# Performance work log

Hardware: AMD Instinct MI355X
Metric: run time of the kernel (lower is better)

The kernel has to match this reference:

```python
import jax, jax.numpy as jnp
import numpy as np

# irreps "64x0e + 32x1o + 16x2e": dims 64*1 + 32*3 + 16*5 = 240
MUL = (64, 32, 16)
DEG = (1, 3, 5)  # 2l+1 for l=0,1,2
IRREPS_DIM = sum(m * d for m, d in zip(MUL, DEG))  # 240
N_NODES = 20000
N_EDGES = 320000


def equivariant_linear(x, W0, W1, W2):
    """e3nn-style linear: per-irrep channel mixing shared across m-components,
    with 1/sqrt(fan_in) path normalization."""
    ws = (W0, W1, W2)
    outs = []
    off = 0
    for (mul, deg, W) in zip(MUL, DEG, ws):
        blk = x[:, off:off + mul * deg].reshape(-1, mul, deg)  # (N, mul, 2l+1)
        y = jnp.einsum('oi,nid->nod', W, blk) / jnp.sqrt(jnp.asarray(mul, x.dtype))
        outs.append(y.reshape(-1, mul * deg))
        off += mul * deg
    return jnp.concatenate(outs, axis=-1)


def setup_inputs() -> dict:
    key = jax.random.key(0)
    k1, k2, k3, k4, k5, k6 = jax.random.split(key, 6)
    messages = jax.random.normal(k1, (N_EDGES, IRREPS_DIM), dtype=jnp.float32)
    edge_index = jax.random.randint(k2, (N_EDGES, 2), 0, N_NODES, dtype=jnp.int64)
    edge_cutoff = jax.random.uniform(k3, (N_EDGES,), dtype=jnp.float32)
    W0 = jax.random.normal(k4, (64, 64), dtype=jnp.float32)
    W1 = jax.random.normal(k5, (32, 32), dtype=jnp.float32)
    W2 = jax.random.normal(k6, (16, 16), dtype=jnp.float32)
    return {"messages": messages, "edge_index": edge_index, "edge_cutoff": edge_cutoff,
            "W0": W0, "W1": W1, "W2": W2, "n_nodes": N_NODES}


def reference(messages, edge_index, edge_cutoff, W0, W1, W2, n_nodes):
    target = edge_index[:, 1]
    weighted = messages * edge_cutoff[:, None]  # fused cutoff multiply
    agg = jax.ops.segment_sum(weighted, target, num_segments=n_nodes)  # (n_nodes, 240)
    return equivariant_linear(agg, W0, W1, W2)
```

## Files before the change

kernel.cpp:

```cpp
#include <hip/hip_runtime.h>

#define IRREPS 240
#define NPB 4

__global__ void histogram_kernel(const int* __restrict__ eidx, int* __restrict__ counts,
                                 int n_edges) {
    int e = blockIdx.x * blockDim.x + threadIdx.x;
    if (e >= n_edges) return;
    int2 p = reinterpret_cast<const int2*>(eidx)[e];
    atomicAdd(&counts[p.y], 1);
}

__global__ void scan_kernel(const int* __restrict__ counts, int* __restrict__ offsets,
                            int* __restrict__ cursor, int n) {
    __shared__ int part[1024];
    int t = threadIdx.x;
    int per = (n + 1023) / 1024;
    int start = t * per;
    int end = min(start + per, n);
    int sum = 0;
    for (int i = start; i < end; ++i) sum += counts[i];
    part[t] = sum;
    __syncthreads();
    for (int off = 1; off < 1024; off <<= 1) {
        int v = (t >= off) ? part[t - off] : 0;
        __syncthreads();
        part[t] += v;
        __syncthreads();
    }
    int run = (t == 0) ? 0 : part[t - 1];
    for (int i = start; i < end; ++i) {
        offsets[i] = run;
        cursor[i] = run;
        run += counts[i];
    }
}

__global__ void fill_kernel(const int* __restrict__ eidx, int* __restrict__ cursor,
                            int* __restrict__ edge_ids, int n_edges) {
    int e = blockIdx.x * blockDim.x + threadIdx.x;
    if (e >= n_edges) return;
    int2 p = reinterpret_cast<const int2*>(eidx)[e];
    int pos = atomicAdd(&cursor[p.y], 1);
    edge_ids[pos] = e;
}

__global__ void gather_linear_kernel(const float* __restrict__ msgs,
                                     const float* __restrict__ cutoff,
                                     const int* __restrict__ edge_ids,
                                     const int* __restrict__ offsets,
                                     const int* __restrict__ counts,
                                     const float* __restrict__ W0,
                                     const float* __restrict__ W1,
                                     const float* __restrict__ W2,
                                     float* __restrict__ out,
                                     int n_nodes) {
    __shared__ float s_node[NPB][IRREPS];

    int t = threadIdx.x;
    int w = t >> 6;
    int lane = t & 63;
    int n = blockIdx.x * NPB + w;

    float4 acc = make_float4(0.f, 0.f, 0.f, 0.f);

    if (n < n_nodes) {
        int beg = offsets[n];
        int cnt = counts[n];
        for (int base = 0; base < cnt; base += 64) {
            int bn = min(64, cnt - base);
            int myeid = 0;
            float myw = 0.f;
            if (lane < bn) {
                myeid = edge_ids[beg + base + lane];
                myw = cutoff[myeid];
            }
            #pragma unroll 8
            for (int j = 0; j < bn; ++j) {
                int e = __shfl(myeid, j);
                float wgt = __shfl(myw, j);
                if (lane < 60) {
                    const float4 m = *reinterpret_cast<const float4*>(
                        msgs + (long long)e * IRREPS + lane * 4);
                    acc.x += m.x * wgt;
                    acc.y += m.y * wgt;
                    acc.z += m.z * wgt;
                    acc.w += m.w * wgt;
                }
            }
        }
    }

    if (lane < 60) {
        *reinterpret_cast<float4*>(&s_node[w][lane * 4]) = acc;
    }
    __syncthreads();

    for (int j = 0; j < NPB; ++j) {
        int nd = blockIdx.x * NPB + j;
        if (nd >= n_nodes) break;
        if (t < IRREPS) {
            const float* s = s_node[j];
            float a = 0.f;
            float res;
            if (t < 64) {
                int o = t;
                #pragma unroll 8
                for (int i = 0; i < 64; ++i) a += W0[o * 64 + i] * s[i];
                res = a * 0.125f;
            } else if (t < 160) {
                int rel = t - 64;
                int o = rel / 3, d = rel % 3;
                #pragma unroll 8
                for (int i = 0; i < 32; ++i) a += W1[o * 32 + i] * s[64 + i * 3 + d];
                res = a * 0.17677669529663687f;
            } else {
                int rel = t - 160;
                int o = rel / 5, d = rel % 5;
                #pragma unroll
                for (int i = 0; i < 16; ++i) a += W2[o * 16 + i] * s[160 + i * 5 + d];
                res = a * 0.25f;
            }
            out[(long long)nd * IRREPS + t] = res;
        }
    }
}

extern "C" void kernel_launch(void* const* d_in, const int* in_sizes, int n_in,
                              void* d_out, int out_size, void* d_ws, size_t ws_size,
                              hipStream_t stream) {
    const float* msgs   = (const float*)d_in[0];
    const int*   eidx   = (const int*)d_in[1];
    const float* cutoff = (const float*)d_in[2];
    const float* W0     = (const float*)d_in[3];
    const float* W1     = (const float*)d_in[4];
    const float* W2     = (const float*)d_in[5];

    int n_edges = in_sizes[0] / IRREPS;
    int n_nodes = out_size / IRREPS;

    int* counts   = (int*)d_ws;
    int* offsets  = counts + n_nodes;
    int* cursor   = offsets + n_nodes;
    int* edge_ids = cursor + n_nodes;

    hipMemsetAsync(counts, 0, (size_t)n_nodes * sizeof(int), stream);

    int block = 256;
    int egrid = (n_edges + block - 1) / block;
    histogram_kernel<<<egrid, block, 0, stream>>>(eidx, counts, n_edges);
    scan_kernel<<<1, 1024, 0, stream>>>(counts, offsets, cursor, n_nodes);
    fill_kernel<<<egrid, block, 0, stream>>>(eidx, cursor, edge_ids, n_edges);

    int ngrid = (n_nodes + NPB - 1) / NPB;
    gather_linear_kernel<<<ngrid, 256, 0, stream>>>(
        msgs, cutoff, edge_ids, offsets, counts, W0, W1, W2, (float*)d_out, n_nodes);
}
```

Before: 183.9 us.

## Pre-permute weighted messages into CSR order as bf16 before reduction

New measurement: 236.2 us. 28.4% more time.

```diff
diff --git a/kernel.cpp b/kernel.cpp
--- a/kernel.cpp
+++ b/kernel.cpp
@@ -1,6 +1,8 @@
 #include <hip/hip_runtime.h>
+#include <hip/hip_bf16.h>
 
 #define IRREPS 240
+#define ROWPAD 256
 #define NPB 4
 
 __global__ void histogram_kernel(const int* __restrict__ eidx, int* __restrict__ counts,
@@ -36,18 +38,43 @@
     }
 }
 
-__global__ void fill_kernel(const int* __restrict__ eidx, int* __restrict__ cursor,
-                            int* __restrict__ edge_ids, int n_edges) {
+__global__ void fill_slot_kernel(const int* __restrict__ eidx, int* __restrict__ cursor,
+                                 int* __restrict__ slot, int n_edges) {
     int e = blockIdx.x * blockDim.x + threadIdx.x;
     if (e >= n_edges) return;
     int2 p = reinterpret_cast<const int2*>(eidx)[e];
-    int pos = atomicAdd(&cursor[p.y], 1);
-    edge_ids[pos] = e;
+    slot[e] = atomicAdd(&cursor[p.y], 1);
 }
 
-__global__ void gather_linear_kernel(const float* __restrict__ msgs,
-                                     const float* __restrict__ cutoff,
-                                     const int* __restrict__ edge_ids,
+__global__ void permute_kernel(const float* __restrict__ msgs,
+                               const float* __restrict__ cutoff,
+                               const int* __restrict__ slot,
+                               __hip_bfloat16* __restrict__ perm,
+                               int n_edges) {
+    int t = threadIdx.x;
+    int w = t >> 6;
+    int lane = t & 63;
+    int e = blockIdx.x * 4 + w;
+    if (e >= n_edges) return;
+
+    int pos = slot[e];
+    float wt = cutoff[e];
+
+    union { __hip_bfloat16 h[4]; uint2 u; } pk;
+    if (lane < 60) {
+        const float4 m = *reinterpret_cast<const float4*>(
+            msgs + (size_t)e * IRREPS + lane * 4);
+        pk.h[0] = __float2bfloat16(m.x * wt);
+        pk.h[1] = __float2bfloat16(m.y * wt);
+        pk.h[2] = __float2bfloat16(m.z * wt);
+        pk.h[3] = __float2bfloat16(m.w * wt);
+    } else {
+        pk.u = make_uint2(0u, 0u);
+    }
+    *reinterpret_cast<uint2*>(perm + (size_t)pos * ROWPAD + lane * 4) = pk.u;
+}
+
+__global__ void reduce_linear_kernel(const __hip_bfloat16* __restrict__ perm,
                                      const int* __restrict__ offsets,
                                      const int* __restrict__ counts,
                                      const float* __restrict__ W0,
@@ -67,31 +94,18 @@
     if (n < n_nodes) {
         int beg = offsets[n];
         int cnt = counts[n];
-        for (int base = 0; base < cnt; base += 64) {
-            int bn = min(64, cnt - base);
-            int myeid = 0;
-            float myw = 0.f;
-            if (lane < bn) {
-                myeid = edge_ids[beg + base + lane];
-                myw = cutoff[myeid];
-            }
-            #pragma unroll 8
-            for (int j = 0; j < bn; ++j) {
-                int e = __shfl(myeid, j);
-                float wgt = __shfl(myw, j);
-                if (lane < 60) {
-                    const float4 m = *reinterpret_cast<const float4*>(
-                        msgs + (long long)e * IRREPS + lane * 4);
-                    acc.x += m.x * wgt;
-                    acc.y += m.y * wgt;
-                    acc.z += m.z * wgt;
-                    acc.w += m.w * wgt;
-                }
-            }
+        const __hip_bfloat16* base = perm + (size_t)beg * ROWPAD + lane * 4;
+        #pragma unroll 8
+        for (int j = 0; j < cnt; ++j) {
+            uint2 u = *reinterpret_cast<const uint2*>(base + (size_t)j * ROWPAD);
+            acc.x += __uint_as_float(u.x << 16);
+            acc.y += __uint_as_float(u.x & 0xffff0000u);
+            acc.z += __uint_as_float(u.y << 16);
+            acc.w += __uint_as_float(u.y & 0xffff0000u);
         }
     }
 
-    if (lane < 60) {
+    if (n < n_nodes && lane < 60) {
         *reinterpret_cast<float4*>(&s_node[w][lane * 4]) = acc;
     }
     __syncthreads();
@@ -121,7 +135,7 @@
                 for (int i = 0; i < 16; ++i) a += W2[o * 16 + i] * s[160 + i * 5 + d];
                 res = a * 0.25f;
             }
-            out[(long long)nd * IRREPS + t] = res;
+            out[(size_t)nd * IRREPS + t] = res;
         }
     }
 }
@@ -139,10 +153,13 @@
     int n_edges = in_sizes[0] / IRREPS;
     int n_nodes = out_size / IRREPS;
 
-    int* counts   = (int*)d_ws;
-    int* offsets  = counts + n_nodes;
-    int* cursor   = offsets + n_nodes;
-    int* edge_ids = cursor + n_nodes;
+    int* counts  = (int*)d_ws;
+    int* offsets = counts + n_nodes;
+    int* cursor  = offsets + n_nodes;
+    int* slot    = cursor + n_nodes;
+    size_t intbytes = ((size_t)3 * n_nodes + (size_t)n_edges) * sizeof(int);
+    size_t permoff = (intbytes + 511) & ~(size_t)511;
+    __hip_bfloat16* perm = (__hip_bfloat16*)((char*)d_ws + permoff);
 
     hipMemsetAsync(counts, 0, (size_t)n_nodes * sizeof(int), stream);
 
@@ -150,9 +167,12 @@
     int egrid = (n_edges + block - 1) / block;
     histogram_kernel<<<egrid, block, 0, stream>>>(eidx, counts, n_edges);
     scan_kernel<<<1, 1024, 0, stream>>>(counts, offsets, cursor, n_nodes);
-    fill_kernel<<<egrid, block, 0, stream>>>(eidx, cursor, edge_ids, n_edges);
+    fill_slot_kernel<<<egrid, block, 0, stream>>>(eidx, cursor, slot, n_edges);
+
+    int pgrid = (n_edges + 3) / 4;
+    permute_kernel<<<pgrid, 256, 0, stream>>>(msgs, cutoff, slot, perm, n_edges);
 
     int ngrid = (n_nodes + NPB - 1) / NPB;
-    gather_linear_kernel<<<ngrid, 256, 0, stream>>>(
-        msgs, cutoff, edge_ids, offsets, counts, W0, W1, W2, (float*)d_out, n_nodes);
+    reduce_linear_kernel<<<ngrid, 256, 0, stream>>>(
+        perm, offsets, counts, W0, W1, W2, (float*)d_out, n_nodes);
 }
```

## Pack edge id with cutoff and interleave two nodes per wave in gather

Applied to the files above, without the earlier changes.

New measurement: 205.5 us. 1.12x slower.

```diff
diff --git a/kernel.cpp b/kernel.cpp
--- a/kernel.cpp
+++ b/kernel.cpp
@@ -1,7 +1,10 @@
 #include <hip/hip_runtime.h>
 
 #define IRREPS 240
-#define NPB 4
+#define WPB 4
+#define NPB 8
+
+typedef float floatx4 __attribute__((ext_vector_type(4)));
 
 __global__ void histogram_kernel(const int* __restrict__ eidx, int* __restrict__ counts,
                                  int n_edges) {
@@ -36,18 +39,20 @@
     }
 }
 
-__global__ void fill_kernel(const int* __restrict__ eidx, int* __restrict__ cursor,
-                            int* __restrict__ edge_ids, int n_edges) {
+__global__ void fill_pairs_kernel(const int* __restrict__ eidx,
+                                  const float* __restrict__ cutoff,
+                                  int* __restrict__ cursor,
+                                  int2* __restrict__ pairs, int n_edges) {
     int e = blockIdx.x * blockDim.x + threadIdx.x;
     if (e >= n_edges) return;
     int2 p = reinterpret_cast<const int2*>(eidx)[e];
+    float w = cutoff[e];
     int pos = atomicAdd(&cursor[p.y], 1);
-    edge_ids[pos] = e;
+    pairs[pos] = make_int2(e, __float_as_int(w));
 }
 
 __global__ void gather_linear_kernel(const float* __restrict__ msgs,
-                                     const float* __restrict__ cutoff,
-                                     const int* __restrict__ edge_ids,
+                                     const int2* __restrict__ pairs,
                                      const int* __restrict__ offsets,
                                      const int* __restrict__ counts,
                                      const float* __restrict__ W0,
@@ -60,39 +65,42 @@
     int t = threadIdx.x;
     int w = t >> 6;
     int lane = t & 63;
-    int n = blockIdx.x * NPB + w;
 
-    float4 acc = make_float4(0.f, 0.f, 0.f, 0.f);
+    int n0 = blockIdx.x * NPB + w;
+    int n1 = n0 + WPB;
 
-    if (n < n_nodes) {
-        int beg = offsets[n];
-        int cnt = counts[n];
-        for (int base = 0; base < cnt; base += 64) {
-            int bn = min(64, cnt - base);
-            int myeid = 0;
-            float myw = 0.f;
-            if (lane < bn) {
-                myeid = edge_ids[beg + base + lane];
-                myw = cutoff[myeid];
+    int b0 = 0, c0 = 0, b1 = 0, c1 = 0;
+    if (n0 < n_nodes) { b0 = offsets[n0]; c0 = counts[n0]; }
+    if (n1 < n_nodes) { b1 = offsets[n1]; c1 = counts[n1]; }
+
+    const floatx4* mp = reinterpret_cast<const floatx4*>(msgs);
+    floatx4 a0 = (floatx4)(0.f);
+    floatx4 a1 = (floatx4)(0.f);
+
+    int jm = max(c0, c1);
+    #pragma unroll 4
+    for (int j = 0; j < jm; ++j) {
+        if (j < c0) {
+            int2 pr = pairs[b0 + j];
+            if (lane < 60) {
+                floatx4 m = __builtin_nontemporal_load(&mp[(size_t)pr.x * 60 + lane]);
+                float wt = __int_as_float(pr.y);
+                a0 += m * wt;
             }
-            #pragma unroll 8
-            for (int j = 0; j < bn; ++j) {
-                int e = __shfl(myeid, j);
-                float wgt = __shfl(myw, j);
-                if (lane < 60) {
-                    const float4 m = *reinterpret_cast<const float4*>(
-                        msgs + (long long)e * IRREPS + lane * 4);
-                    acc.x += m.x * wgt;
-                    acc.y += m.y * wgt;
-                    acc.z += m.z * wgt;
-                    acc.w += m.w * wgt;
-                }
+        }
+        if (j < c1) {
+            int2 pr = pairs[b1 + j];
+            if (lane < 60) {
+                floatx4 m = __builtin_nontemporal_load(&mp[(size_t)pr.x * 60 + lane]);
+                float wt = __int_as_float(pr.y);
+                a1 += m * wt;
             }
         }
     }
 
     if (lane < 60) {
-        *reinterpret_cast<float4*>(&s_node[w][lane * 4]) = acc;
+        *reinterpret_cast<floatx4*>(&s_node[w][lane * 4]) = a0;
+        *reinterpret_cast<floatx4*>(&s_node[w + WPB][lane * 4]) = a1;
     }
     __syncthreads();
 
@@ -110,18 +118,18 @@
                 res = a * 0.125f;
             } else if (t < 160) {
                 int rel = t - 64;
-                int o = rel / 3, d = rel % 3;
+                int o = rel / 3, d = rel - o * 3;
                 #pragma unroll 8
                 for (int i = 0; i < 32; ++i) a += W1[o * 32 + i] * s[64 + i * 3 + d];
                 res = a * 0.17677669529663687f;
             } else {
                 int rel = t - 160;
-                int o = rel / 5, d = rel % 5;
+                int o = rel / 5, d = rel - o * 5;
                 #pragma unroll
                 for (int i = 0; i < 16; ++i) a += W2[o * 16 + i] * s[160 + i * 5 + d];
                 res = a * 0.25f;
             }
-            out[(long long)nd * IRREPS + t] = res;
+            out[(size_t)nd * IRREPS + t] = res;
         }
     }
 }
@@ -139,20 +147,20 @@
     int n_edges = in_sizes[0] / IRREPS;
     int n_nodes = out_size / IRREPS;
 
-    int* counts   = (int*)d_ws;
-    int* offsets  = counts + n_nodes;
-    int* cursor   = offsets + n_nodes;
-    int* edge_ids = cursor + n_nodes;
+    int*  counts  = (int*)d_ws;
+    int*  offsets = counts + n_nodes;
+    int*  cursor  = offsets + n_nodes;
+    int2* pairs   = (int2*)(cursor + n_nodes);
 
-    hipMemsetAsync(counts, 0, (size_t)n_nodes * sizeof(int), stream);
+    (void)hipMemsetAsync(counts, 0, (size_t)n_nodes * sizeof(int), stream);
 
     int block = 256;
     int egrid = (n_edges + block - 1) / block;
     histogram_kernel<<<egrid, block, 0, stream>>>(eidx, counts, n_edges);
     scan_kernel<<<1, 1024, 0, stream>>>(counts, offsets, cursor, n_nodes);
-    fill_kernel<<<egrid, block, 0, stream>>>(eidx, cursor, edge_ids, n_edges);
+    fill_pairs_kernel<<<egrid, block, 0, stream>>>(eidx, cutoff, cursor, pairs, n_edges);
 
     int ngrid = (n_nodes + NPB - 1) / NPB;
     gather_linear_kernel<<<ngrid, 256, 0, stream>>>(
-        msgs, cutoff, edge_ids, offsets, counts, W0, W1, W2, (float*)d_out, n_nodes);
+        msgs, pairs, offsets, counts, W0, W1, W2, (float*)d_out, n_nodes);
 }
```
